# Kernel optimization log

Hardware: AMD Instinct MI355X
Metric: run time of the kernel (lower is better)

The kernel has to match this reference:

```python
import jax, jax.numpy as jnp
import numpy as np

MARGIN = 1.0  # init kwarg margin
EPS = 1e-16


def setup_inputs() -> dict:
    key = jax.random.key(0)
    k1, k2 = jax.random.split(key)
    embeddings = jax.random.normal(k1, (512, 128), dtype=jnp.float32)
    labels = jax.random.randint(k2, (512,), 0, 32)
    return {"embeddings": embeddings, "labels": labels}


def _pairwise_l2(e):
    # exact p=2 cdist via explicit differences; safe sqrt so grad at d=0 is 0
    diff = e[:, None, :] - e[None, :, :]          # [N, N, D]
    sq = jnp.sum(diff * diff, axis=-1)             # [N, N]
    safe = jnp.where(sq > 0, sq, 1.0)
    return jnp.where(sq > 0, jnp.sqrt(safe), 0.0)


def reference(embeddings, labels):
    # _batch_all_triplet_loss (default mining_type='online_hard_negative')
    n = labels.shape[0]
    d = _pairwise_l2(embeddings)                   # [N, N]

    not_eye = ~jnp.eye(n, dtype=bool)
    # distinct (i, j, k) triplets
    distinct = not_eye[:, :, None] & not_eye[:, None, :] & not_eye[None, :, :]
    label_eq = labels[:, None] == labels[None, :]  # symmetric [N, N]
    # labels[i] == labels[j] and labels[i] != labels[k]
    mask = label_eq[:, :, None] & (~label_eq[:, None, :]) & distinct  # [N, N, N]

    # d(a, p) - d(a, n) + margin, masked and hinged
    triplet_loss = mask.astype(d.dtype) * (d[:, :, None] - d[:, None, :] + MARGIN)
    triplet_loss = jnp.maximum(triplet_loss, 0.0)

    n_positive = jnp.sum(triplet_loss > EPS).astype(d.dtype)
    n_triplets = jnp.sum(mask).astype(d.dtype)
    fraction_positive = n_positive / (n_triplets + EPS)
    loss = jnp.sum(triplet_loss) / (n_positive + EPS)
    return loss, fraction_positive
```

## Files before the change

### kernel.cpp

```cpp
#include <hip/hip_runtime.h>

constexpr int N = 512;
constexpr int D = 128;
constexpr int A = 2;
constexpr int NBLK = N / A;
constexpr float MARGIN = 1.0f;
constexpr float EPS_T = 1e-16f;

__global__ __launch_bounds__(512, 2) void triplet_main_k(
    const float* __restrict__ emb, const int* __restrict__ labels,
    double* __restrict__ partial)
{
    __shared__ float  drow[A][N];
    __shared__ float  posd[A][N];
    __shared__ int    cnt[A][8];
    __shared__ int    npos_s[A];
    __shared__ double red[24];

    const int i0   = blockIdx.x * A;
    const int tid  = threadIdx.x;
    const int lane = tid & 63;
    const int wid  = tid >> 6;
    const int sub  = tid & 7;

    const float4* ea0 = reinterpret_cast<const float4*>(emb + (size_t)i0 * D);
    const float4* ea1 = reinterpret_cast<const float4*>(emb + (size_t)(i0 + 1) * D);
    const float4 a00 = ea0[sub], a01 = ea0[sub + 8], a02 = ea0[sub + 16], a03 = ea0[sub + 24];
    const float4 a10 = ea1[sub], a11 = ea1[sub + 8], a12 = ea1[sub + 16], a13 = ea1[sub + 24];

    const int lk  = labels[tid];
    const int li0 = labels[i0];
    const int li1 = labels[i0 + 1];

    #pragma unroll
    for (int p = 0; p < 8; ++p) {
        const int r = p * 64 + (tid >> 3);
        const float4* er = reinterpret_cast<const float4*>(emb + (size_t)r * D);
        const float4 v0 = er[sub], v1 = er[sub + 8], v2 = er[sub + 16], v3 = er[sub + 24];
        float sq0 = 0.f, sq1 = 0.f;
        {
            float d0 = a00.x - v0.x, d1 = a00.y - v0.y, d2 = a00.z - v0.z, d3 = a00.w - v0.w;
            sq0 += d0 * d0 + d1 * d1 + d2 * d2 + d3 * d3;
            d0 = a01.x - v1.x; d1 = a01.y - v1.y; d2 = a01.z - v1.z; d3 = a01.w - v1.w;
            sq0 += d0 * d0 + d1 * d1 + d2 * d2 + d3 * d3;
            d0 = a02.x - v2.x; d1 = a02.y - v2.y; d2 = a02.z - v2.z; d3 = a02.w - v2.w;
            sq0 += d0 * d0 + d1 * d1 + d2 * d2 + d3 * d3;
            d0 = a03.x - v3.x; d1 = a03.y - v3.y; d2 = a03.z - v3.z; d3 = a03.w - v3.w;
            sq0 += d0 * d0 + d1 * d1 + d2 * d2 + d3 * d3;
        }
        {
            float d0 = a10.x - v0.x, d1 = a10.y - v0.y, d2 = a10.z - v0.z, d3 = a10.w - v0.w;
            sq1 += d0 * d0 + d1 * d1 + d2 * d2 + d3 * d3;
            d0 = a11.x - v1.x; d1 = a11.y - v1.y; d2 = a11.z - v1.z; d3 = a11.w - v1.w;
            sq1 += d0 * d0 + d1 * d1 + d2 * d2 + d3 * d3;
            d0 = a12.x - v2.x; d1 = a12.y - v2.y; d2 = a12.z - v2.z; d3 = a12.w - v2.w;
            sq1 += d0 * d0 + d1 * d1 + d2 * d2 + d3 * d3;
            d0 = a13.x - v3.x; d1 = a13.y - v3.y; d2 = a13.z - v3.z; d3 = a13.w - v3.w;
            sq1 += d0 * d0 + d1 * d1 + d2 * d2 + d3 * d3;
        }
        sq0 += __shfl_xor(sq0, 1); sq1 += __shfl_xor(sq1, 1);
        sq0 += __shfl_xor(sq0, 2); sq1 += __shfl_xor(sq1, 2);
        sq0 += __shfl_xor(sq0, 4); sq1 += __shfl_xor(sq1, 4);
        if (sub == 0) {
            drow[0][r] = (sq0 > 0.f) ? sqrtf(sq0) : 0.f;
            drow[1][r] = (sq1 > 0.f) ? sqrtf(sq1) : 0.f;
        }
    }
    __syncthreads();

    const int j = wid * 64 + lane;
    const bool p0 = (labels[j] == li0) && (j != i0);
    const bool p1 = (labels[j] == li1) && (j != i0 + 1);
    const unsigned long long m0 = __ballot(p0);
    const unsigned long long m1 = __ballot(p1);
    if (lane == 0) { cnt[0][wid] = __popcll(m0); cnt[1][wid] = __popcll(m1); }
    __syncthreads();
    int base0 = 0, base1 = 0;
    for (int w = 0; w < 8; ++w) {
        const int c0 = cnt[0][w], c1 = cnt[1][w];
        base0 += (w < wid) ? c0 : 0;
        base1 += (w < wid) ? c1 : 0;
    }
    if (p0) posd[0][base0 + __popcll(m0 & ((1ull << lane) - 1ull))] = drow[0][j];
    if (p1) posd[1][base1 + __popcll(m1 & ((1ull << lane) - 1ull))] = drow[1][j];
    if (tid == 0) {
        int t0 = 0, t1 = 0;
        #pragma unroll
        for (int w = 0; w < 8; ++w) { t0 += cnt[0][w]; t1 += cnt[1][w]; }
        npos_s[0] = t0; npos_s[1] = t1;
    }
    __syncthreads();

    double sum = 0.0;
    int np_i = 0, nt_i = 0;
    {
        const float dik = drow[0][tid];
        if (lk != li0) {
            const int npos = npos_s[0];
            #pragma unroll 4
            for (int p = 0; p < npos; ++p) {
                const float t = (posd[0][p] - dik) + MARGIN;
                if (t > EPS_T) { sum += (double)t; ++np_i; }
            }
            nt_i += npos;
        }
    }
    {
        const float dik = drow[1][tid];
        if (lk != li1) {
            const int npos = npos_s[1];
            #pragma unroll 4
            for (int p = 0; p < npos; ++p) {
                const float t = (posd[1][p] - dik) + MARGIN;
                if (t > EPS_T) { sum += (double)t; ++np_i; }
            }
            nt_i += npos;
        }
    }

    double s = sum, p = (double)np_i, t = (double)nt_i;
    #pragma unroll
    for (int off = 32; off > 0; off >>= 1) {
        s += __shfl_down(s, off);
        p += __shfl_down(p, off);
        t += __shfl_down(t, off);
    }
    if (lane == 0) { red[wid] = s; red[8 + wid] = p; red[16 + wid] = t; }
    __syncthreads();
    if (tid == 0) {
        double S = 0.0, P = 0.0, T = 0.0;
        #pragma unroll
        for (int w = 0; w < 8; ++w) { S += red[w]; P += red[8 + w]; T += red[16 + w]; }
        partial[blockIdx.x]            = S;
        partial[NBLK + blockIdx.x]     = P;
        partial[2 * NBLK + blockIdx.x] = T;
    }
}

__global__ __launch_bounds__(256) void triplet_final_k(
    const double* __restrict__ partial, float* __restrict__ out)
{
    __shared__ double red[12];
    const int tid  = threadIdx.x;
    const int lane = tid & 63;
    const int wid  = tid >> 6;
    double a = partial[tid];
    double b = partial[NBLK + tid];
    double c = partial[2 * NBLK + tid];
    #pragma unroll
    for (int off = 32; off > 0; off >>= 1) {
        a += __shfl_down(a, off);
        b += __shfl_down(b, off);
        c += __shfl_down(c, off);
    }
    if (lane == 0) { red[wid] = a; red[4 + wid] = b; red[8 + wid] = c; }
    __syncthreads();
    if (tid == 0) {
        const double S = red[0] + red[1] + red[2]  + red[3];
        const double P = red[4] + red[5] + red[6]  + red[7];
        const double T = red[8] + red[9] + red[10] + red[11];
        out[0] = (float)(S / (P + 1e-16));
        out[1] = (float)(P / (T + 1e-16));
    }
}

extern "C" void kernel_launch(void* const* d_in, const int* in_sizes, int n_in,
                              void* d_out, int out_size, void* d_ws, size_t ws_size,
                              hipStream_t stream) {
    const float* emb   = (const float*)d_in[0];
    const int*   lab   = (const int*)d_in[1];
    float*       out   = (float*)d_out;
    double*      parts = (double*)d_ws;

    triplet_main_k<<<NBLK, 512, 0, stream>>>(emb, lab, parts);
    triplet_final_k<<<1, 256, 0, stream>>>(parts, out);
}
```

Baseline: 15.36 us.

## Restructure triplet kernel to compute positive distances first and split positive loop across lanes

Builds a compact list of positive indices per anchor before computing any distances. It then computes anchor-positive distances only for those rows and fuses the anchor-negative distance computation with the hinge loop. The per-negative loop over positives is spread across 8 sub-lanes instead of one thread per negative, which reduces serial inner-loop length. It adds a second distance pass and caps positives at 64 per anchor, which holds only if no class has more than 64 members. The final reduction uses one wavefront over an interleaved partial layout.

```diff
diff --git a/kernel.cpp b/kernel.cpp
--- a/kernel.cpp
+++ b/kernel.cpp
@@ -11,10 +11,11 @@
     const float* __restrict__ emb, const int* __restrict__ labels,
     double* __restrict__ partial)
 {
-    __shared__ float  drow[A][N];
-    __shared__ float  posd[A][N];
-    __shared__ int    cnt[A][8];
-    __shared__ int    npos_s[A];
+    __shared__ int    lab[N];
+    __shared__ int    plist[2 * 64];
+    __shared__ float  posd[2][64];
+    __shared__ int    cnt[2][8];
+    __shared__ int    npos_s[2];
     __shared__ double red[24];
 
     const int i0   = blockIdx.x * A;
@@ -22,67 +23,34 @@
     const int lane = tid & 63;
     const int wid  = tid >> 6;
     const int sub  = tid & 7;
+    const int grp  = tid >> 3;
 
     const float4* ea0 = reinterpret_cast<const float4*>(emb + (size_t)i0 * D);
     const float4* ea1 = reinterpret_cast<const float4*>(emb + (size_t)(i0 + 1) * D);
     const float4 a00 = ea0[sub], a01 = ea0[sub + 8], a02 = ea0[sub + 16], a03 = ea0[sub + 24];
     const float4 a10 = ea1[sub], a11 = ea1[sub + 8], a12 = ea1[sub + 16], a13 = ea1[sub + 24];
 
-    const int lk  = labels[tid];
+    lab[tid] = labels[tid];
     const int li0 = labels[i0];
     const int li1 = labels[i0 + 1];
-
-    #pragma unroll
-    for (int p = 0; p < 8; ++p) {
-        const int r = p * 64 + (tid >> 3);
-        const float4* er = reinterpret_cast<const float4*>(emb + (size_t)r * D);
-        const float4 v0 = er[sub], v1 = er[sub + 8], v2 = er[sub + 16], v3 = er[sub + 24];
-        float sq0 = 0.f, sq1 = 0.f;
-        {
-            float d0 = a00.x - v0.x, d1 = a00.y - v0.y, d2 = a00.z - v0.z, d3 = a00.w - v0.w;
-            sq0 += d0 * d0 + d1 * d1 + d2 * d2 + d3 * d3;
-            d0 = a01.x - v1.x; d1 = a01.y - v1.y; d2 = a01.z - v1.z; d3 = a01.w - v1.w;
-            sq0 += d0 * d0 + d1 * d1 + d2 * d2 + d3 * d3;
-            d0 = a02.x - v2.x; d1 = a02.y - v2.y; d2 = a02.z - v2.z; d3 = a02.w - v2.w;
-            sq0 += d0 * d0 + d1 * d1 + d2 * d2 + d3 * d3;
-            d0 = a03.x - v3.x; d1 = a03.y - v3.y; d2 = a03.z - v3.z; d3 = a03.w - v3.w;
-            sq0 += d0 * d0 + d1 * d1 + d2 * d2 + d3 * d3;
-        }
-        {
-            float d0 = a10.x - v0.x, d1 = a10.y - v0.y, d2 = a10.z - v0.z, d3 = a10.w - v0.w;
-            sq1 += d0 * d0 + d1 * d1 + d2 * d2 + d3 * d3;
-            d0 = a11.x - v1.x; d1 = a11.y - v1.y; d2 = a11.z - v1.z; d3 = a11.w - v1.w;
-            sq1 += d0 * d0 + d1 * d1 + d2 * d2 + d3 * d3;
-            d0 = a12.x - v2.x; d1 = a12.y - v2.y; d2 = a12.z - v2.z; d3 = a12.w - v2.w;
-            sq1 += d0 * d0 + d1 * d1 + d2 * d2 + d3 * d3;
-            d0 = a13.x - v3.x; d1 = a13.y - v3.y; d2 = a13.z - v3.z; d3 = a13.w - v3.w;
-            sq1 += d0 * d0 + d1 * d1 + d2 * d2 + d3 * d3;
-        }
-        sq0 += __shfl_xor(sq0, 1); sq1 += __shfl_xor(sq1, 1);
-        sq0 += __shfl_xor(sq0, 2); sq1 += __shfl_xor(sq1, 2);
-        sq0 += __shfl_xor(sq0, 4); sq1 += __shfl_xor(sq1, 4);
-        if (sub == 0) {
-            drow[0][r] = (sq0 > 0.f) ? sqrtf(sq0) : 0.f;
-            drow[1][r] = (sq1 > 0.f) ? sqrtf(sq1) : 0.f;
-        }
-    }
-    __syncthreads();
-
-    const int j = wid * 64 + lane;
-    const bool p0 = (labels[j] == li0) && (j != i0);
-    const bool p1 = (labels[j] == li1) && (j != i0 + 1);
+    __syncthreads();
+
+    const int j = tid;
+    const bool p0 = (lab[j] == li0) && (j != i0);
+    const bool p1 = (lab[j] == li1) && (j != i0 + 1);
     const unsigned long long m0 = __ballot(p0);
     const unsigned long long m1 = __ballot(p1);
     if (lane == 0) { cnt[0][wid] = __popcll(m0); cnt[1][wid] = __popcll(m1); }
     __syncthreads();
     int base0 = 0, base1 = 0;
+    #pragma unroll
     for (int w = 0; w < 8; ++w) {
-        const int c0 = cnt[0][w], c1 = cnt[1][w];
-        base0 += (w < wid) ? c0 : 0;
-        base1 += (w < wid) ? c1 : 0;
-    }
-    if (p0) posd[0][base0 + __popcll(m0 & ((1ull << lane) - 1ull))] = drow[0][j];
-    if (p1) posd[1][base1 + __popcll(m1 & ((1ull << lane) - 1ull))] = drow[1][j];
+        base0 += (w < wid) ? cnt[0][w] : 0;
+        base1 += (w < wid) ? cnt[1][w] : 0;
+    }
+    const unsigned long long lm = (1ull << lane) - 1ull;
+    if (p0) plist[base0 + __popcll(m0 & lm)]      = j;
+    if (p1) plist[64 + base1 + __popcll(m1 & lm)] = j;
     if (tid == 0) {
         int t0 = 0, t1 = 0;
         #pragma unroll
@@ -91,30 +59,91 @@
     }
     __syncthreads();
 
+    const int np0 = npos_s[0];
+    const int np1 = npos_s[1];
+
+    for (int e = grp; e < np0 + np1; e += 64) {
+        const int  a   = (e < np0) ? 0 : 1;
+        const int  idx = (e < np0) ? e : (e - np0);
+        const int  row = plist[a * 64 + idx];
+        const float4* er = reinterpret_cast<const float4*>(emb + (size_t)row * D);
+        const float4 v0 = er[sub], v1 = er[sub + 8], v2 = er[sub + 16], v3 = er[sub + 24];
+        float sq0 = 0.f, sq1 = 0.f;
+        {
+            float d0 = a00.x - v0.x, d1 = a00.y - v0.y, d2 = a00.z - v0.z, d3 = a00.w - v0.w;
+            sq0 += d0 * d0 + d1 * d1 + d2 * d2 + d3 * d3;
+            d0 = a01.x - v1.x; d1 = a01.y - v1.y; d2 = a01.z - v1.z; d3 = a01.w - v1.w;
+            sq0 += d0 * d0 + d1 * d1 + d2 * d2 + d3 * d3;
+            d0 = a02.x - v2.x; d1 = a02.y - v2.y; d2 = a02.z - v2.z; d3 = a02.w - v2.w;
+            sq0 += d0 * d0 + d1 * d1 + d2 * d2 + d3 * d3;
+            d0 = a03.x - v3.x; d1 = a03.y - v3.y; d2 = a03.z - v3.z; d3 = a03.w - v3.w;
+            sq0 += d0 * d0 + d1 * d1 + d2 * d2 + d3 * d3;
+        }
+        {
+            float d0 = a10.x - v0.x, d1 = a10.y - v0.y, d2 = a10.z - v0.z, d3 = a10.w - v0.w;
+            sq1 += d0 * d0 + d1 * d1 + d2 * d2 + d3 * d3;
+            d0 = a11.x - v1.x; d1 = a11.y - v1.y; d2 = a11.z - v1.z; d3 = a11.w - v1.w;
+            sq1 += d0 * d0 + d1 * d1 + d2 * d2 + d3 * d3;
+            d0 = a12.x - v2.x; d1 = a12.y - v2.y; d2 = a12.z - v2.z; d3 = a12.w - v2.w;
+            sq1 += d0 * d0 + d1 * d1 + d2 * d2 + d3 * d3;
+            d0 = a13.x - v3.x; d1 = a13.y - v3.y; d2 = a13.z - v3.z; d3 = a13.w - v3.w;
+            sq1 += d0 * d0 + d1 * d1 + d2 * d2 + d3 * d3;
+        }
+        sq0 += __shfl_xor(sq0, 1); sq1 += __shfl_xor(sq1, 1);
+        sq0 += __shfl_xor(sq0, 2); sq1 += __shfl_xor(sq1, 2);
+        sq0 += __shfl_xor(sq0, 4); sq1 += __shfl_xor(sq1, 4);
+        const float sq = (e < np0) ? sq0 : sq1;
+        if (sub == 0) posd[a][idx] = (sq > 0.f) ? sqrtf(sq) : 0.f;
+    }
+    __syncthreads();
+
     double sum = 0.0;
     int np_i = 0, nt_i = 0;
-    {
-        const float dik = drow[0][tid];
-        if (lk != li0) {
-            const int npos = npos_s[0];
-            #pragma unroll 4
-            for (int p = 0; p < npos; ++p) {
-                const float t = (posd[0][p] - dik) + MARGIN;
+    #pragma unroll 2
+    for (int p = 0; p < 8; ++p) {
+        const int r = p * 64 + grp;
+        const float4* er = reinterpret_cast<const float4*>(emb + (size_t)r * D);
+        const float4 v0 = er[sub], v1 = er[sub + 8], v2 = er[sub + 16], v3 = er[sub + 24];
+        float sq0 = 0.f, sq1 = 0.f;
+        {
+            float d0 = a00.x - v0.x, d1 = a00.y - v0.y, d2 = a00.z - v0.z, d3 = a00.w - v0.w;
+            sq0 += d0 * d0 + d1 * d1 + d2 * d2 + d3 * d3;
+            d0 = a01.x - v1.x; d1 = a01.y - v1.y; d2 = a01.z - v1.z; d3 = a01.w - v1.w;
+            sq0 += d0 * d0 + d1 * d1 + d2 * d2 + d3 * d3;
+            d0 = a02.x - v2.x; d1 = a02.y - v2.y; d2 = a02.z - v2.z; d3 = a02.w - v2.w;
+            sq0 += d0 * d0 + d1 * d1 + d2 * d2 + d3 * d3;
+            d0 = a03.x - v3.x; d1 = a03.y - v3.y; d2 = a03.z - v3.z; d3 = a03.w - v3.w;
+            sq0 += d0 * d0 + d1 * d1 + d2 * d2 + d3 * d3;
+        }
+        {
+            float d0 = a10.x - v0.x, d1 = a10.y - v0.y, d2 = a10.z - v0.z, d3 = a10.w - v0.w;
+            sq1 += d0 * d0 + d1 * d1 + d2 * d2 + d3 * d3;
+            d0 = a11.x - v1.x; d1 = a11.y - v1.y; d2 = a11.z - v1.z; d3 = a11.w - v1.w;
+            sq1 += d0 * d0 + d1 * d1 + d2 * d2 + d3 * d3;
+            d0 = a12.x - v2.x; d1 = a12.y - v2.y; d2 = a12.z - v2.z; d3 = a12.w - v2.w;
+            sq1 += d0 * d0 + d1 * d1 + d2 * d2 + d3 * d3;
+            d0 = a13.x - v3.x; d1 = a13.y - v3.y; d2 = a13.z - v3.z; d3 = a13.w - v3.w;
+            sq1 += d0 * d0 + d1 * d1 + d2 * d2 + d3 * d3;
+        }
+        sq0 += __shfl_xor(sq0, 1); sq1 += __shfl_xor(sq1, 1);
+        sq0 += __shfl_xor(sq0, 2); sq1 += __shfl_xor(sq1, 2);
+        sq0 += __shfl_xor(sq0, 4); sq1 += __shfl_xor(sq1, 4);
+        const float dk0 = (sq0 > 0.f) ? sqrtf(sq0) : 0.f;
+        const float dk1 = (sq1 > 0.f) ? sqrtf(sq1) : 0.f;
+        const int   lr  = lab[r];
+        if (lr != li0) {
+            for (int q = sub; q < np0; q += 8) {
+                const float t = (posd[0][q] - dk0) + MARGIN;
+                ++nt_i;
                 if (t > EPS_T) { sum += (double)t; ++np_i; }
             }
-            nt_i += npos;
-        }
-    }
-    {
-        const float dik = drow[1][tid];
-        if (lk != li1) {
-            const int npos = npos_s[1];
-            #pragma unroll 4
-            for (int p = 0; p < npos; ++p) {
-                const float t = (posd[1][p] - dik) + MARGIN;
+        }
+        if (lr != li1) {
+            for (int q = sub; q < np1; q += 8) {
+                const float t = (posd[1][q] - dk1) + MARGIN;
+                ++nt_i;
                 if (t > EPS_T) { sum += (double)t; ++np_i; }
             }
-            nt_i += npos;
         }
     }
 
@@ -131,36 +160,32 @@
         double S = 0.0, P = 0.0, T = 0.0;
         #pragma unroll
         for (int w = 0; w < 8; ++w) { S += red[w]; P += red[8 + w]; T += red[16 + w]; }
-        partial[blockIdx.x]            = S;
-        partial[NBLK + blockIdx.x]     = P;
-        partial[2 * NBLK + blockIdx.x] = T;
+        partial[4 * blockIdx.x + 0] = S;
+        partial[4 * blockIdx.x + 1] = P;
+        partial[4 * blockIdx.x + 2] = T;
     }
 }
 
-__global__ __launch_bounds__(256) void triplet_final_k(
+__global__ __launch_bounds__(64) void triplet_final_k(
     const double* __restrict__ partial, float* __restrict__ out)
 {
-    __shared__ double red[12];
-    const int tid  = threadIdx.x;
-    const int lane = tid & 63;
-    const int wid  = tid >> 6;
-    double a = partial[tid];
-    double b = partial[NBLK + tid];
-    double c = partial[2 * NBLK + tid];
+    const int lane = threadIdx.x;
+    double a = 0.0, b = 0.0, c = 0.0;
+    #pragma unroll
+    for (int bk = lane; bk < NBLK; bk += 64) {
+        a += partial[4 * bk + 0];
+        b += partial[4 * bk + 1];
+        c += partial[4 * bk + 2];
+    }
     #pragma unroll
     for (int off = 32; off > 0; off >>= 1) {
         a += __shfl_down(a, off);
         b += __shfl_down(b, off);
         c += __shfl_down(c, off);
     }
-    if (lane == 0) { red[wid] = a; red[4 + wid] = b; red[8 + wid] = c; }
-    __syncthreads();
-    if (tid == 0) {
-        const double S = red[0] + red[1] + red[2]  + red[3];
-        const double P = red[4] + red[5] + red[6]  + red[7];
-        const double T = red[8] + red[9] + red[10] + red[11];
-        out[0] = (float)(S / (P + 1e-16));
-        out[1] = (float)(P / (T + 1e-16));
+    if (lane == 0) {
+        out[0] = (float)(a / (b + 1e-16));
+        out[1] = (float)(b / (c + 1e-16));
     }
 }
 
@@ -173,5 +198,5 @@
     double*      parts = (double*)d_ws;
 
     triplet_main_k<<<NBLK, 512, 0, stream>>>(emb, lab, parts);
-    triplet_final_k<<<1, 256, 0, stream>>>(parts, out);
+    triplet_final_k<<<1, 64, 0, stream>>>(parts, out);
 }
```

Measured after the change: 19.49 us. +26.9%, slower.
